# Kernel optimization log

Measured on AMD Instinct MI355X. Metric: run time of the kernel, lower is better.

## Reference

```python
import jax, jax.numpy as jnp
import numpy as np

# Hyperparameters matching the torch module instantiation
STRIDE = (2, 2, 2)
PADDING = (1, 1, 1)
OUTPUT_PADDING = (1, 1, 1)
DILATION = (2, 2, 2)
KERNEL = (3, 3, 3)


def setup_inputs() -> dict:
    key = jax.random.key(0)
    k1, k2, k3 = jax.random.split(key, 3)
    x = jax.random.normal(k1, (2, 64, 32, 32, 32), dtype=jnp.float32)
    # torch ConvTranspose3d weight layout: (C_in, C_out//groups, kD, kH, kW)
    weight = jax.random.normal(k2, (64, 32, 3, 3, 3), dtype=jnp.float32) * 0.05
    bias = jax.random.normal(k3, (32,), dtype=jnp.float32) * 0.05
    return {"x": x, "weight": weight, "bias": bias}


def reference(x, weight, bias):
    # Same math as the naive torch module: zero-insertion upsample by stride,
    # symmetric pad by dilation*(k-1)-padding, dense conv3d with the spatially
    # flipped weight at rhs dilation, trailing output_padding, then bias add.
    # lhs_dilation performs the zero-insertion implicitly (identical result).
    pad = tuple(max(0, d * (k - 1) - p)
                for d, k, p in zip(DILATION, KERNEL, PADDING))
    # (C_in, C_out, k,k,k) -> (C_out, C_in, k,k,k), flipped spatially
    w = jnp.flip(jnp.transpose(weight, (1, 0, 2, 3, 4)), axis=(2, 3, 4))
    out = jax.lax.conv_general_dilated(
        x, w,
        window_strides=(1, 1, 1),
        padding=[(p, p) for p in pad],
        lhs_dilation=STRIDE,
        rhs_dilation=DILATION,
        dimension_numbers=("NCDHW", "OIDHW", "NCDHW"),
    )
    opd, oph, opw = OUTPUT_PADDING
    out = jnp.pad(out, ((0, 0), (0, 0), (0, opd), (0, oph), (0, opw)))
    return out + bias[None, :, None, None, None]
```

## Files before the change

kernel.cpp:

```cpp
#include <hip/hip_runtime.h>


#define DOUT 66
#define PL (DOUT*DOUT)

typedef _Float16 half8 __attribute__((ext_vector_type(8)));
typedef float    floatx16 __attribute__((ext_vector_type(16)));

#define X16_N_F16  2228224
#define ROW_B      4352
#define ZSLAB_OFF  112640
#define X16_OFF    131072

#define PB_W    216
#define PB_X    512
#define PB_B    579
#define PREP_GRID (PB_W + PB_X + PB_B)

__global__ void __launch_bounds__(256) prep(
    const float* __restrict__ x, const float* __restrict__ w,
    const float* __restrict__ bias, _Float16* __restrict__ wA,
    _Float16* __restrict__ x16, uint4* __restrict__ zslab,
    float* __restrict__ out)
{
    const int tid = threadIdx.x;
    unsigned b = blockIdx.x;

    if (b < PB_W) {
        int o = b * 256 + tid;
        int j = o & 7;
        int tmp = o >> 3;
        int lane = tmp & 63;
        int g = tmp >> 6;
        int cc = g / 27, tap = g - cc * 27;
        int co = lane & 31, khalf = lane >> 5;
        int ci = cc * 16 + khalf * 8 + j;
        wA[o] = (_Float16)w[ci * 864 + co * 27 + tap];
        return;
    }
    b -= PB_W;
    if (b < PB_X) {
        const int id = b & 31;
        const int q2 = (b >> 5) & 7;
        const int n  = b >> 8;
        const int iw = tid & 31;
        const int cihalf = (tid >> 5) & 1;
        const int ihq = tid >> 6;
        const int ih = q2 * 4 + ihq;

        if (b == 0) {
            zslab[2 * tid]     = make_uint4(0, 0, 0, 0);
            zslab[2 * tid + 1] = make_uint4(0, 0, 0, 0);
        }

        const float* xr = x + (size_t)n * 2097152 + (id * 32 + ih) * 32 + iw;
        _Float16* drow = x16 + (size_t)n * X16_N_F16 + (id * 32 + ih) * 2176;
        const int c0 = cihalf * 32;

        float f[32];
        #pragma unroll
        for (int j = 0; j < 32; ++j) f[j] = xr[(size_t)(c0 + j) * 32768];
        #pragma unroll
        for (int k = 0; k < 4; ++k) {
            unsigned pk[4];
            #pragma unroll
            for (int j = 0; j < 4; ++j)
                pk[j] = __builtin_bit_cast(unsigned,
                    __builtin_amdgcn_cvt_pkrtz(f[8 * k + 2 * j], f[8 * k + 2 * j + 1]));
            const int ccg = cihalf * 4 + k;
            *(uint4*)(drow + ccg * 272 + (iw + 1) * 8) =
                make_uint4(pk[0], pk[1], pk[2], pk[3]);
        }
        if (tid < 64) {
            const int ihq2 = tid >> 4;
            const int rem  = tid & 15;
            const int ccg  = rem >> 1, side = rem & 1;
            _Float16* hz = x16 + (size_t)n * X16_N_F16 +
                (id * 32 + q2 * 4 + ihq2) * 2176 + ccg * 272 + (side ? 264 : 0);
            *(uint4*)hz = make_uint4(0, 0, 0, 0);
        }
        return;
    }
    b -= PB_X;
    {
        const unsigned base = b * 4096u;
        #pragma unroll
        for (int j = 0; j < 16; ++j) {
            unsigned g = base + j * 256u + tid;
            if (g >= 2369952u) continue;
            unsigned pl = g / 1089u;
            unsigned slot = g - pl * 1089u;
            unsigned e  = pl % 34u;
            unsigned nc = pl / 34u;
            unsigned od = (e < 33u) ? 2u * e : 65u;
            float v = bias[nc & 31u];
            float4* p = (float4*)(out + ((size_t)nc * DOUT + od) * PL);
            p[slot] = make_float4(v, v, v, v);
        }
    }
}

__global__ void __launch_bounds__(256, 3) convt(
    const _Float16* __restrict__ x16, const _Float16* __restrict__ wA,
    const _Float16* __restrict__ zslab, const float* __restrict__ bias,
    float* __restrict__ out)
{
    __shared__ __align__(16) unsigned char xlds[52224];

    const int tid  = threadIdx.x;
    const int lane = tid & 63;
    const int wv   = tid >> 6;

    unsigned b = blockIdx.x;
    const unsigned xcd = b & 7u;
    const int n   = xcd & 1;
    const unsigned rest = b >> 3;
    const int dp  = rest & 31;
    const int hq2 = rest >> 5;
    const int hpg = (int)((xcd >> 1) * 4 + hq2);
    const int hpb = hpg * 2;

    const char* xby = (const char*)(x16 + (size_t)n * X16_N_F16);
    const char* zby = (const char*)zslab;
    for (int m = wv; m < 51; m += 4) {
        int c = m * 64 + lane;
        int r = c >> 8;
        r = c / 272;
        int q = c - r * 272;
        int idl = r >> 2, ihl = r & 3;
        int id = dp - 1 + idl, ih = hpb - 1 + ihl;
        bool v = ((unsigned)id < 32u) & ((unsigned)ih < 32u);
        const char* g = v ? (xby + (id * 32 + ih) * ROW_B + q * 16) : (zby + q * 16);
        __builtin_amdgcn_global_load_lds(
            (const __attribute__((address_space(1))) void*)g,
            (__attribute__((address_space(3))) void*)(xlds + m * 1024),
            16, 0, 0);
    }

    uint4 A[27];
    const _Float16* wl = wA + ((size_t)wv * 27 * 64 + lane) * 8;
    #pragma unroll
    for (int t = 0; t < 27; ++t) A[t] = *(const uint4*)(wl + t * 512);

    __syncthreads();

    const int wp    = lane & 31;
    const int khalf = lane >> 5;
    const int cbase = (2 * wv + khalf) * 544 + wp * 16;

    floatx16 acc0 = {}, acc1 = {};
    #pragma unroll
    for (int kd = 0; kd < 3; ++kd)
    #pragma unroll
    for (int kh = 0; kh < 3; ++kh)
    #pragma unroll
    for (int kw = 0; kw < 3; ++kw) {
        const int tap = (kd * 3 + kh) * 3 + kw;
        const int row0 = (2 - kd) * 4 + (2 - kh);
        const uint4* bp0 = (const uint4*)(xlds + row0 * ROW_B + cbase + (2 - kw) * 16);
        acc0 = __builtin_amdgcn_mfma_f32_32x32x16_f16(
            __builtin_bit_cast(half8, A[tap]),
            __builtin_bit_cast(half8, bp0[0]), acc0, 0, 0, 0);
        const uint4* bp1 = (const uint4*)((const char*)bp0 + ROW_B);
        acc1 = __builtin_amdgcn_mfma_f32_32x32x16_f16(
            __builtin_bit_cast(half8, A[tap]),
            __builtin_bit_cast(half8, bp1[0]), acc1, 0, 0, 0);
    }

    __syncthreads();
    float* part = (float*)xlds;
    if (wv != 0) {
        #pragma unroll
        for (int r = 0; r < 16; ++r)
            part[((wv * 2 + 0) * 16 + r) * 64 + lane] = acc0[r];
    }
    if (wv != 1) {
        #pragma unroll
        for (int r = 0; r < 16; ++r)
            part[((wv * 2 + 1) * 16 + r) * 64 + lane] = acc1[r];
    }
    __syncthreads();

    const int od = 2 * dp + 1;
    if (wv <= 1) {
        float s[16];
        #pragma unroll
        for (int r = 0; r < 16; ++r) {
            s[r] = (wv == 0) ? acc0[r] : acc1[r];
            #pragma unroll
            for (int w2 = 0; w2 < 4; ++w2) {
                if (w2 == wv) continue;
                s[r] += part[((w2 * 2 + wv) * 16 + r) * 64 + lane];
            }
        }
        const int oh = 2 * (hpb + wv) + 1;
        #pragma unroll
        for (int r = 0; r < 16; ++r) {
            const int co = (r & 3) + 8 * (r >> 2) + 4 * khalf;
            const float bv = bias[co];
            float2* orow = (float2*)(out +
                ((size_t)(n * 32 + co) * DOUT + od) * PL + oh * DOUT);
            orow[wp] = make_float2(bv, s[r] + bv);
            if (wp == 31) orow[32] = make_float2(bv, bv);
        }
    } else {
        const int oh = (wv == 2) ? 2 * hpb : 2 * hpb + 2;
        const int oht = (wv == 2) ? 64 : 65;
        const bool tails = (hpg == 15);
        #pragma unroll
        for (int r = 0; r < 16; ++r) {
            const int co = (r & 3) + 8 * (r >> 2) + 4 * khalf;
            const float bv = bias[co];
            float* pbase = out + ((size_t)(n * 32 + co) * DOUT + od) * PL;
            float2* erow = (float2*)(pbase + oh * DOUT);
            erow[wp] = make_float2(bv, bv);
            if (wp == 31) erow[32] = make_float2(bv, bv);
            if (tails) {
                float2* trow = (float2*)(pbase + oht * DOUT);
                trow[wp] = make_float2(bv, bv);
                if (wp == 31) trow[32] = make_float2(bv, bv);
            }
        }
    }
}

extern "C" void kernel_launch(void* const* d_in, const int* in_sizes, int n_in,
                              void* d_out, int out_size, void* d_ws, size_t ws_size,
                              hipStream_t stream) {
    const float* x    = (const float*)d_in[0];
    const float* wgt  = (const float*)d_in[1];
    const float* bias = (const float*)d_in[2];
    float* out = (float*)d_out;
    _Float16* wA    = (_Float16*)d_ws;
    uint4*    zslab = (uint4*)((char*)d_ws + ZSLAB_OFF);
    _Float16* x16   = (_Float16*)((char*)d_ws + X16_OFF);

    prep<<<PREP_GRID, 256, 0, stream>>>(x, wgt, bias, wA, x16, zslab, out);
    convt<<<1024, 256, 0, stream>>>(x16, wA, (const _Float16*)zslab, bias, out);
}
```

Baseline: 108.6 us.

## Fuse fp32-to-fp16 input conversion and bias plane fill into conv kernel

Drops the separate x16 staging buffer: the conv kernel now reads fp32 input directly, converts it to fp16 and writes it into LDS, zero-filling padding. The bias-only even-depth planes are written by the idle waves of the conv kernel, no longer by the prep kernel, and output stores use nontemporal hints. This removes a full fp16 round trip through global memory and shrinks prep to weights only. In exchange each input row is re-read and re-converted by the neighbouring blocks that share it (about 3x redundancy), and the direct-to-LDS async loads are replaced by register-staged loads.

```diff
diff --git a/kernel.cpp b/kernel.cpp
--- a/kernel.cpp
+++ b/kernel.cpp
@@ -3,107 +3,30 @@
 
 #define DOUT 66
 #define PL (DOUT*DOUT)
-
-typedef _Float16 half8 __attribute__((ext_vector_type(8)));
+#define ROW_B 4352
+
+typedef _Float16 half8   __attribute__((ext_vector_type(8)));
 typedef float    floatx16 __attribute__((ext_vector_type(16)));
-
-#define X16_N_F16  2228224
-#define ROW_B      4352
-#define ZSLAB_OFF  112640
-#define X16_OFF    131072
-
-#define PB_W    216
-#define PB_X    512
-#define PB_B    579
-#define PREP_GRID (PB_W + PB_X + PB_B)
-
-__global__ void __launch_bounds__(256) prep(
-    const float* __restrict__ x, const float* __restrict__ w,
-    const float* __restrict__ bias, _Float16* __restrict__ wA,
-    _Float16* __restrict__ x16, uint4* __restrict__ zslab,
-    float* __restrict__ out)
+typedef float    floatx4  __attribute__((ext_vector_type(4)));
+typedef float    floatx2  __attribute__((ext_vector_type(2)));
+
+__global__ void __launch_bounds__(256) wprep(const float* __restrict__ w,
+                                             _Float16* __restrict__ wA)
 {
-    const int tid = threadIdx.x;
-    unsigned b = blockIdx.x;
-
-    if (b < PB_W) {
-        int o = b * 256 + tid;
-        int j = o & 7;
-        int tmp = o >> 3;
-        int lane = tmp & 63;
-        int g = tmp >> 6;
-        int cc = g / 27, tap = g - cc * 27;
-        int co = lane & 31, khalf = lane >> 5;
-        int ci = cc * 16 + khalf * 8 + j;
-        wA[o] = (_Float16)w[ci * 864 + co * 27 + tap];
-        return;
-    }
-    b -= PB_W;
-    if (b < PB_X) {
-        const int id = b & 31;
-        const int q2 = (b >> 5) & 7;
-        const int n  = b >> 8;
-        const int iw = tid & 31;
-        const int cihalf = (tid >> 5) & 1;
-        const int ihq = tid >> 6;
-        const int ih = q2 * 4 + ihq;
-
-        if (b == 0) {
-            zslab[2 * tid]     = make_uint4(0, 0, 0, 0);
-            zslab[2 * tid + 1] = make_uint4(0, 0, 0, 0);
-        }
-
-        const float* xr = x + (size_t)n * 2097152 + (id * 32 + ih) * 32 + iw;
-        _Float16* drow = x16 + (size_t)n * X16_N_F16 + (id * 32 + ih) * 2176;
-        const int c0 = cihalf * 32;
-
-        float f[32];
-        #pragma unroll
-        for (int j = 0; j < 32; ++j) f[j] = xr[(size_t)(c0 + j) * 32768];
-        #pragma unroll
-        for (int k = 0; k < 4; ++k) {
-            unsigned pk[4];
-            #pragma unroll
-            for (int j = 0; j < 4; ++j)
-                pk[j] = __builtin_bit_cast(unsigned,
-                    __builtin_amdgcn_cvt_pkrtz(f[8 * k + 2 * j], f[8 * k + 2 * j + 1]));
-            const int ccg = cihalf * 4 + k;
-            *(uint4*)(drow + ccg * 272 + (iw + 1) * 8) =
-                make_uint4(pk[0], pk[1], pk[2], pk[3]);
-        }
-        if (tid < 64) {
-            const int ihq2 = tid >> 4;
-            const int rem  = tid & 15;
-            const int ccg  = rem >> 1, side = rem & 1;
-            _Float16* hz = x16 + (size_t)n * X16_N_F16 +
-                (id * 32 + q2 * 4 + ihq2) * 2176 + ccg * 272 + (side ? 264 : 0);
-            *(uint4*)hz = make_uint4(0, 0, 0, 0);
-        }
-        return;
-    }
-    b -= PB_X;
-    {
-        const unsigned base = b * 4096u;
-        #pragma unroll
-        for (int j = 0; j < 16; ++j) {
-            unsigned g = base + j * 256u + tid;
-            if (g >= 2369952u) continue;
-            unsigned pl = g / 1089u;
-            unsigned slot = g - pl * 1089u;
-            unsigned e  = pl % 34u;
-            unsigned nc = pl / 34u;
-            unsigned od = (e < 33u) ? 2u * e : 65u;
-            float v = bias[nc & 31u];
-            float4* p = (float4*)(out + ((size_t)nc * DOUT + od) * PL);
-            p[slot] = make_float4(v, v, v, v);
-        }
-    }
+    int o = blockIdx.x * 256 + threadIdx.x;
+    int j = o & 7;
+    int tmp = o >> 3;
+    int lane = tmp & 63;
+    int g = tmp >> 6;
+    int cc = g / 27, tap = g - cc * 27;
+    int co = lane & 31, khalf = lane >> 5;
+    int ci = cc * 16 + khalf * 8 + j;
+    wA[o] = (_Float16)w[ci * 864 + co * 27 + tap];
 }
 
 __global__ void __launch_bounds__(256, 3) convt(
-    const _Float16* __restrict__ x16, const _Float16* __restrict__ wA,
-    const _Float16* __restrict__ zslab, const float* __restrict__ bias,
-    float* __restrict__ out)
+    const float* __restrict__ x, const _Float16* __restrict__ wA,
+    const float* __restrict__ bias, float* __restrict__ out)
 {
     __shared__ __align__(16) unsigned char xlds[52224];
 
@@ -113,28 +36,56 @@
 
     unsigned b = blockIdx.x;
     const unsigned xcd = b & 7u;
-    const int n   = xcd & 1;
+    const int n   = (int)(xcd & 1u);
     const unsigned rest = b >> 3;
-    const int dp  = rest & 31;
-    const int hq2 = rest >> 5;
+    const int dp  = (int)(rest & 31u);
+    const int hq2 = (int)(rest >> 5);
     const int hpg = (int)((xcd >> 1) * 4 + hq2);
     const int hpb = hpg * 2;
 
-    const char* xby = (const char*)(x16 + (size_t)n * X16_N_F16);
-    const char* zby = (const char*)zslab;
-    for (int m = wv; m < 51; m += 4) {
-        int c = m * 64 + lane;
-        int r = c >> 8;
-        r = c / 272;
-        int q = c - r * 272;
-        int idl = r >> 2, ihl = r & 3;
-        int id = dp - 1 + idl, ih = hpb - 1 + ihl;
-        bool v = ((unsigned)id < 32u) & ((unsigned)ih < 32u);
-        const char* g = v ? (xby + (id * 32 + ih) * ROW_B + q * 16) : (zby + q * 16);
-        __builtin_amdgcn_global_load_lds(
-            (const __attribute__((address_space(1))) void*)g,
-            (__attribute__((address_space(3))) void*)(xlds + m * 1024),
-            16, 0, 0);
+    const float* xn = x + (size_t)n * 2097152;
+    const int gq  = tid & 7;
+    const int ccg = (tid >> 3) & 7;
+    #pragma unroll
+    for (int k = 0; k < 3; ++k) {
+        const int r  = k * 4 + wv;
+        const int id = dp  - 1 + (r >> 2);
+        const int ih = hpb - 1 + (r & 3);
+        unsigned char* dst = xlds + r * ROW_B + ccg * 544 + (gq * 4 + 1) * 16;
+        if (((unsigned)id < 32u) & ((unsigned)ih < 32u)) {
+            const float* src = xn + ccg * 262144 + (id * 32 + ih) * 32 + gq * 4;
+            floatx4 f0 = *(const floatx4*)(src);
+            floatx4 f1 = *(const floatx4*)(src + 32768);
+            floatx4 f2 = *(const floatx4*)(src + 2 * 32768);
+            floatx4 f3 = *(const floatx4*)(src + 3 * 32768);
+            floatx4 f4 = *(const floatx4*)(src + 4 * 32768);
+            floatx4 f5 = *(const floatx4*)(src + 5 * 32768);
+            floatx4 f6 = *(const floatx4*)(src + 6 * 32768);
+            floatx4 f7 = *(const floatx4*)(src + 7 * 32768);
+            #pragma unroll
+            for (int m = 0; m < 4; ++m) {
+                unsigned p0 = __builtin_bit_cast(unsigned,
+                    __builtin_amdgcn_cvt_pkrtz(f0[m], f1[m]));
+                unsigned p1 = __builtin_bit_cast(unsigned,
+                    __builtin_amdgcn_cvt_pkrtz(f2[m], f3[m]));
+                unsigned p2 = __builtin_bit_cast(unsigned,
+                    __builtin_amdgcn_cvt_pkrtz(f4[m], f5[m]));
+                unsigned p3 = __builtin_bit_cast(unsigned,
+                    __builtin_amdgcn_cvt_pkrtz(f6[m], f7[m]));
+                *(uint4*)(dst + m * 16) = make_uint4(p0, p1, p2, p3);
+            }
+        } else {
+            #pragma unroll
+            for (int m = 0; m < 4; ++m)
+                *(uint4*)(dst + m * 16) = make_uint4(0, 0, 0, 0);
+        }
+    }
+    if (tid < 192) {
+        const int r   = tid >> 4;
+        const int rem = tid & 15;
+        const int cg  = rem >> 1, side = rem & 1;
+        *(uint4*)(xlds + r * ROW_B + cg * 544 + (side ? 33 * 16 : 0)) =
+            make_uint4(0, 0, 0, 0);
     }
 
     uint4 A[27];
@@ -155,7 +106,7 @@
     for (int kh = 0; kh < 3; ++kh)
     #pragma unroll
     for (int kw = 0; kw < 3; ++kw) {
-        const int tap = (kd * 3 + kh) * 3 + kw;
+        const int tap  = (kd * 3 + kh) * 3 + kw;
         const int row0 = (2 - kd) * 4 + (2 - kh);
         const uint4* bp0 = (const uint4*)(xlds + row0 * ROW_B + cbase + (2 - kw) * 16);
         acc0 = __builtin_amdgcn_mfma_f32_32x32x16_f16(
@@ -198,27 +149,50 @@
         for (int r = 0; r < 16; ++r) {
             const int co = (r & 3) + 8 * (r >> 2) + 4 * khalf;
             const float bv = bias[co];
-            float2* orow = (float2*)(out +
+            floatx2* orow = (floatx2*)(out +
                 ((size_t)(n * 32 + co) * DOUT + od) * PL + oh * DOUT);
-            orow[wp] = make_float2(bv, s[r] + bv);
-            if (wp == 31) orow[32] = make_float2(bv, bv);
+            floatx2 vv = {bv, s[r] + bv};
+            __builtin_nontemporal_store(vv, orow + wp);
+            if (wp == 31) {
+                floatx2 bb2 = {bv, bv};
+                __builtin_nontemporal_store(bb2, orow + 32);
+            }
         }
     } else {
-        const int oh = (wv == 2) ? 2 * hpb : 2 * hpb + 2;
-        const int oht = (wv == 2) ? 64 : 65;
         const bool tails = (hpg == 15);
+        const bool extra = (dp == 31);
+        const int ohA = (wv == 2) ? 2 * hpb : 2 * hpb + 2;
+        const int ohT = (wv == 2) ? 64 : 65;
+        const int e0  = 4 * hpg + ((wv == 2) ? 0 : 2);
+        auto putrow = [&](float* plane, int oh, floatx2 bb) {
+            floatx2* rw = (floatx2*)(plane + oh * DOUT);
+            __builtin_nontemporal_store(bb, rw + wp);
+            if (wp == 31) __builtin_nontemporal_store(bb, rw + 32);
+        };
         #pragma unroll
         for (int r = 0; r < 16; ++r) {
             const int co = (r & 3) + 8 * (r >> 2) + 4 * khalf;
             const float bv = bias[co];
-            float* pbase = out + ((size_t)(n * 32 + co) * DOUT + od) * PL;
-            float2* erow = (float2*)(pbase + oh * DOUT);
-            erow[wp] = make_float2(bv, bv);
-            if (wp == 31) erow[32] = make_float2(bv, bv);
-            if (tails) {
-                float2* trow = (float2*)(pbase + oht * DOUT);
-                trow[wp] = make_float2(bv, bv);
-                if (wp == 31) trow[32] = make_float2(bv, bv);
+            const floatx2 bb = {bv, bv};
+            float* pc    = out + (size_t)(n * 32 + co) * ((size_t)DOUT * PL);
+            float* podd  = pc + (size_t)od * PL;
+            float* peven = pc + (size_t)(od - 1) * PL;
+            putrow(podd, ohA, bb);
+            if (tails) putrow(podd, ohT, bb);
+            putrow(peven, e0, bb);
+            putrow(peven, e0 + 1, bb);
+            if (tails) putrow(peven, ohT, bb);
+            if (extra) {
+                float* p64 = pc + (size_t)64 * PL;
+                float* p65 = pc + (size_t)65 * PL;
+                putrow(p64, e0, bb);
+                putrow(p64, e0 + 1, bb);
+                putrow(p65, e0, bb);
+                putrow(p65, e0 + 1, bb);
+                if (tails) {
+                    putrow(p64, ohT, bb);
+                    putrow(p65, ohT, bb);
+                }
             }
         }
     }
@@ -231,10 +205,8 @@
     const float* wgt  = (const float*)d_in[1];
     const float* bias = (const float*)d_in[2];
     float* out = (float*)d_out;
-    _Float16* wA    = (_Float16*)d_ws;
-    uint4*    zslab = (uint4*)((char*)d_ws + ZSLAB_OFF);
-    _Float16* x16   = (_Float16*)((char*)d_ws + X16_OFF);
-
-    prep<<<PREP_GRID, 256, 0, stream>>>(x, wgt, bias, wA, x16, zslab, out);
-    convt<<<1024, 256, 0, stream>>>(x16, wA, (const _Float16*)zslab, bias, out);
+    _Float16* wA = (_Float16*)d_ws;
+
+    wprep<<<216, 256, 0, stream>>>(wgt, wA);
+    convt<<<1024, 256, 0, stream>>>(x, wA, bias, out);
 }
```

Result: slower. 125.0 us (+15.1%).
